# Kernel tuning notes

Hardware: AMD Instinct MI355X
Metric: run time of the kernel (lower is better)

## Reference

```python
import jax, jax.numpy as jnp
import numpy as np

B, S, HID = 8, 1024, 1024
NH, HD = 16, 64  # num heads, head dim; NH*HD == HID


def setup_inputs() -> dict:
    key = jax.random.key(0)
    ks = jax.random.split(key, 8)
    sc = 0.02
    return {
        "hidden_states": jax.random.normal(ks[0], (B, S, HID), jnp.float32),
        "attention_mask": jnp.zeros((B, 1, 1, S), jnp.float32),
        "Wq": jax.random.normal(ks[1], (HID, HID), jnp.float32) * sc,
        "bq": jnp.zeros((HID,), jnp.float32),
        "Wk": jax.random.normal(ks[2], (HID, HID), jnp.float32) * sc,
        "bk": jnp.zeros((HID,), jnp.float32),
        "Wv": jax.random.normal(ks[3], (HID, HID), jnp.float32) * sc,
        "bv": jnp.zeros((HID,), jnp.float32),
    }


def reference(hidden_states, attention_mask, Wq, bq, Wk, bk, Wv, bv):
    def split_heads(x):  # [B,S,HID] -> [B,NH,S,HD]
        return x.reshape(B, S, NH, HD).transpose(0, 2, 1, 3)

    q = split_heads(hidden_states @ Wq + bq)
    k = split_heads(hidden_states @ Wk + bk)
    v = split_heads(hidden_states @ Wv + bv)

    # [B,NH,S,S] score matrix, scale, additive mask, softmax
    scores = jnp.einsum("bhqd,bhkd->bhqk", q, k) / jnp.sqrt(jnp.float32(HD))
    scores = scores + attention_mask
    probs = jax.nn.softmax(scores, axis=-1)  # dropout prob = 0.0 -> identity

    ctx = jnp.einsum("bhqk,bhkd->bhqd", probs, v)
    return ctx.transpose(0, 2, 1, 3).reshape(B, S, HID)
```

## Files before the change

kernel.cpp:

```cpp
#include <hip/hip_runtime.h>


typedef __bf16 bf16x8 __attribute__((ext_vector_type(8)));
typedef float f32x4 __attribute__((ext_vector_type(4)));
typedef float f32x16 __attribute__((ext_vector_type(16)));
typedef int i32x4 __attribute__((ext_vector_type(4)));

__device__ __forceinline__ unsigned rne16(float x) {
  unsigned u = __builtin_bit_cast(unsigned, x);
  return (u + 0x7fffu + ((u >> 16) & 1u)) >> 16;
}
__device__ __forceinline__ unsigned packbf(float lo, float hi) {
  return rne16(lo) | (rne16(hi) << 16);
}
__device__ __forceinline__ unsigned packbf_fast(float lo, float hi) {
  unsigned ul = __builtin_bit_cast(unsigned, lo) + 0x8000u;
  unsigned uh = __builtin_bit_cast(unsigned, hi) + 0x8000u;
  return __builtin_amdgcn_perm(uh, ul, 0x07060302u);
}
__device__ __forceinline__ void async16(void* l, const void* g) {
  __builtin_amdgcn_global_load_lds((const __attribute__((address_space(1))) void*)g,
                                   (__attribute__((address_space(3))) void*)l, 16, 0, 0);
}
__device__ __forceinline__ bf16x8 dsr128(const char* p) {
  i32x4 r;
  unsigned a = (unsigned)(size_t)(const __attribute__((address_space(3))) char*)p;
  asm volatile("ds_read_b128 %0, %1" : "=v"(r) : "v"(a));
  return __builtin_bit_cast(bf16x8, r);
}

__global__ __launch_bounds__(256) void k_prep(const float* __restrict__ h,
                                              unsigned short* __restrict__ hbf,
                                              const float* __restrict__ Wq,
                                              const float* __restrict__ Wk,
                                              const float* __restrict__ Wv,
                                              unsigned short* __restrict__ wt) {
  __shared__ float t[32][33];
  int bid = blockIdx.x, tid = threadIdx.x;
  if (bid < 8192) {
    size_t i = (size_t)bid * 256 + tid;
    float4 v = ((const float4*)h)[i];
    uint2 r;
    r.x = packbf(v.x, v.y);
    r.y = packbf(v.z, v.w);
    ((uint2*)hbf)[i] = r;
  } else {
    int id = bid - 8192;
    int which = id >> 10;
    int sub = id & 1023;
    int c0 = (sub & 31) * 32, k0 = (sub >> 5) * 32;
    const float* W = which == 0 ? Wq : (which == 1 ? Wk : Wv);
    int tx = tid & 31, ty = tid >> 5;
#pragma unroll
    for (int i = 0; i < 4; ++i) {
      int r = ty + i * 8;
      t[r][tx] = W[(size_t)(k0 + r) * 1024 + c0 + tx];
    }
    __syncthreads();
#pragma unroll
    for (int i = 0; i < 4; ++i) {
      int r = ty + i * 8;
      wt[((size_t)which * 1024 + c0 + r) * 1024 + k0 + tx] = (unsigned short)rne16(t[tx][r]);
    }
  }
}

__global__ __launch_bounds__(512, 2) void k_gemm(const unsigned short* __restrict__ A,
                                                 const unsigned short* __restrict__ Bm,
                                                 const float* __restrict__ bq,
                                                 const float* __restrict__ bk,
                                                 const float* __restrict__ bv,
                                                 unsigned short* __restrict__ qkv,
                                                 unsigned short* __restrict__ vt) {
  __shared__ __align__(16) char lds[147456];
  const int tid = threadIdx.x;
  const int w = tid >> 6, lane = tid & 63;
  const int wm = w >> 1, wn = w & 1;

  int orig = blockIdx.x;
  int wgid = (orig & 7) * 96 + (orig >> 3);
  int tm = wgid / 24, tn = wgid - tm * 24;
  int m0 = tm * 256, n0 = tn * 128;

  int ro[2], ke[2];
#pragma unroll
  for (int j = 0; j < 2; ++j) {
    int o = j * 8192 + tid * 16;
    int s = o >> 10, w10 = o & 1023;
    int lg = w10 ^ (((w10 >> 9) & 1) << 5);
    ro[j] = ((s >> 1) << 4) + (lg >> 6);
    ke[j] = ((s & 1) << 5) + ((lg & 63) >> 1);
  }
  auto stage_half = [&](int ldsoff, const unsigned short* src, int rb, int k0) {
#pragma unroll
    for (int j = 0; j < 2; ++j)
      async16(lds + ldsoff + j * 8192 + w * 1024,
              src + (size_t)(rb + ro[j]) * 1024 + (k0 + ke[j]));
  };
  auto stAB = [&](int t, int doff) {
    stage_half(doff, A, m0, t * 64);
    stage_half(doff + 16384, A, m0 + 128, t * 64);
    stage_half(doff + 32768, Bm, n0, t * 64);
  };

  const int lswz = (((lane & 15) << 6) | ((lane >> 4) << 4)) ^ ((lane & 8) << 2);

  f32x4 acc[4][4];
#pragma unroll
  for (int i = 0; i < 4; ++i)
#pragma unroll
    for (int j = 0; j < 4; ++j)
#pragma unroll
      for (int e = 0; e < 4; ++e) acc[i][j][e] = 0.f;

  stAB(0, 0);
  stAB(1, 49152);
  asm volatile("s_waitcnt vmcnt(6)");
  __builtin_amdgcn_s_barrier();
  __builtin_amdgcn_sched_barrier(0);

  int cur = 0;
#pragma unroll 1
  for (int kt = 0; kt < 16; ++kt) {
    const char* buf = lds + cur * 49152;
    int nxt2 = cur + 2; if (nxt2 >= 3) nxt2 -= 3;
    const char* abase = buf + (wm >> 1) * 16384 + lswz;
    const char* bbase = buf + 32768 + lswz;
    bf16x8 aF[4][2], bF[4][2];
#pragma unroll
    for (int n = 0; n < 4; ++n)
      bF[n][0] = dsr128(bbase + ((wn * 4 + n) * 2 + 0) * 1024);
#pragma unroll
    for (int mt = 0; mt < 4; ++mt)
      aF[mt][0] = dsr128(abase + (((wm & 1) * 4 + mt) * 2 + 0) * 1024);
    if (kt < 14) stAB(kt + 2, nxt2 * 49152);
#pragma unroll
    for (int n = 0; n < 4; ++n)
      bF[n][1] = dsr128(bbase + ((wn * 4 + n) * 2 + 1) * 1024);
#pragma unroll
    for (int mt = 0; mt < 4; ++mt)
      aF[mt][1] = dsr128(abase + (((wm & 1) * 4 + mt) * 2 + 1) * 1024);
    asm volatile("s_waitcnt lgkmcnt(8)");
    __builtin_amdgcn_sched_barrier(0);
    __builtin_amdgcn_s_setprio(1);
#pragma unroll
    for (int mt = 0; mt < 4; ++mt)
#pragma unroll
      for (int n = 0; n < 4; ++n)
        acc[mt][n] = __builtin_amdgcn_mfma_f32_16x16x32_bf16(aF[mt][0], bF[n][0],
                                                             acc[mt][n], 0, 0, 0);
    __builtin_amdgcn_s_setprio(0);
    asm volatile("s_waitcnt lgkmcnt(0)");
    __builtin_amdgcn_sched_barrier(0);
    __builtin_amdgcn_s_setprio(1);
#pragma unroll
    for (int mt = 0; mt < 4; ++mt)
#pragma unroll
      for (int n = 0; n < 4; ++n)
        acc[mt][n] = __builtin_amdgcn_mfma_f32_16x16x32_bf16(aF[mt][1], bF[n][1],
                                                             acc[mt][n], 0, 0, 0);
    __builtin_amdgcn_s_setprio(0);
    if (kt < 14) asm volatile("s_waitcnt vmcnt(6)");
    else if (kt == 14) asm volatile("s_waitcnt vmcnt(0)");
    if (kt < 15) {
      __builtin_amdgcn_s_barrier();
      __builtin_amdgcn_sched_barrier(0);
    }
    cur = cur + 1; if (cur == 3) cur = 0;
  }

  const int which = tn >> 3;
  const int ng = n0 & 1023;
  const int b = m0 >> 10;
  const int r = lane & 15, qq = lane >> 4;
  const int sb = (m0 & 1023) + wm * 64 + qq * 4;

  if (which != 2) {
    const float* bp = which == 0 ? bq : bk;
    unsigned short* base = qkv + ((size_t)which << 23) + ((size_t)b << 20);
#pragma unroll
    for (int n = 0; n < 4; ++n) {
      int n_in = ng + wn * 64 + n * 16 + r;
      float bias = bp[n_in];
      unsigned short* dp = base + ((size_t)(n_in >> 6) << 16) + (n_in & 63);
#pragma unroll
      for (int m = 0; m < 4; ++m)
#pragma unroll
        for (int e = 0; e < 4; ++e)
          dp[(size_t)(sb + m * 16 + e) << 6] = (unsigned short)rne16(acc[m][n][e] + bias);
    }
  } else {
    unsigned short* vbase = vt + ((size_t)b << 20);
#pragma unroll
    for (int n = 0; n < 4; ++n) {
      int n_in = ng + wn * 64 + n * 16 + r;
      float bias = bv[n_in];
      unsigned short* dp = vbase + ((size_t)n_in << 10) + sb;
#pragma unroll
      for (int m = 0; m < 4; ++m) {
        uint2 pk;
        pk.x = packbf(acc[m][n][0] + bias, acc[m][n][1] + bias);
        pk.y = packbf(acc[m][n][2] + bias, acc[m][n][3] + bias);
        *(uint2*)(dp + m * 16) = pk;
      }
    }
  }
}

__global__ __launch_bounds__(256, 4) void k_attn(const unsigned short* __restrict__ qg,
                                                 const unsigned short* __restrict__ kg,
                                                 const unsigned short* __restrict__ vtg,
                                                 const float* __restrict__ maskg,
                                                 float* __restrict__ out) {
  __shared__ __align__(16) char lds[36864];
  char* KF = lds;
  char* VF = lds + 16384;
  float* MK = (float*)(lds + 32768);
  int tid = threadIdx.x, w = tid >> 6, lane = tid & 63, l5 = lane & 31, q5 = lane >> 5;
  int idx = blockIdx.x;
  int bi = idx & 7;
  int j = idx >> 3;
  int h = j >> 3, qc = j & 7;
  int bh = bi * 16 + h, s0 = qc * 128;
  const unsigned short* qb = qg + ((size_t)bh << 16);
  const unsigned short* kb = kg + ((size_t)bh << 16);
  const unsigned short* vb = vtg + ((size_t)bh << 16);
  const float LG = 1.4426950408889634f;
  const float C1 = 0.125f * LG;

  {
    float4 mv = *(const float4*)(maskg + (size_t)bi * 1024 + tid * 4);
    mv.x *= LG; mv.y *= LG; mv.z *= LG; mv.w *= LG;
    *(float4*)(MK + tid * 4) = mv;
  }

  bf16x8 qfr[4];
#pragma unroll
  for (int ds = 0; ds < 4; ++ds)
    qfr[ds] = *(const bf16x8*)(qb + (size_t)(s0 + w * 32 + l5) * 64 + ds * 16 + q5 * 8);

  f32x16 O[2];
#pragma unroll
  for (int i = 0; i < 2; ++i)
#pragma unroll
    for (int e = 0; e < 16; ++e) O[i][e] = 0.f;
  float lsum = 0.f;

#pragma unroll 1
  for (int kt = 0; kt < 8; ++kt) {
    int k0 = kt * 128;
    __syncthreads();
#pragma unroll
    for (int t = 0; t < 4; ++t) {
      int f = w * 4 + t, mt = f >> 2, ds = f & 3;
      async16(KF + f * 1024, kb + (size_t)(k0 + mt * 32 + l5) * 64 + ds * 16 + q5 * 8);
    }
#pragma unroll
    for (int t = 0; t < 4; ++t) {
      int f = w * 4 + t, dt = f >> 3, ks = f & 7;
      async16(VF + f * 1024, vb + (size_t)(dt * 32 + l5) * 1024 + k0 + ks * 16 + q5 * 8);
    }
    __syncthreads();

#pragma unroll
    for (int mt = 0; mt < 4; ++mt) {
      f32x16 S;
#pragma unroll
      for (int e = 0; e < 16; ++e) S[e] = 0.f;
#pragma unroll
      for (int ds = 0; ds < 4; ++ds) {
        bf16x8 a = *(const bf16x8*)(KF + (mt * 4 + ds) * 1024 + lane * 16);
        S = __builtin_amdgcn_mfma_f32_32x32x16_bf16(a, qfr[ds], S, 0, 0, 0);
      }
      float p[16];
#pragma unroll
      for (int g4 = 0; g4 < 4; ++g4) {
        float4 mv = *(const float4*)(MK + k0 + mt * 32 + g4 * 8 + q5 * 4);
        p[g4 * 4 + 0] = __builtin_amdgcn_exp2f(S[g4 * 4 + 0] * C1 + mv.x);
        p[g4 * 4 + 1] = __builtin_amdgcn_exp2f(S[g4 * 4 + 1] * C1 + mv.y);
        p[g4 * 4 + 2] = __builtin_amdgcn_exp2f(S[g4 * 4 + 2] * C1 + mv.z);
        p[g4 * 4 + 3] = __builtin_amdgcn_exp2f(S[g4 * 4 + 3] * C1 + mv.w);
      }
      unsigned p2[8];
#pragma unroll
      for (int e = 0; e < 16; ++e) lsum += p[e];
#pragma unroll
      for (int jj = 0; jj < 8; ++jj) p2[jj] = packbf_fast(p[2 * jj], p[2 * jj + 1]);
#pragma unroll
      for (int kh = 0; kh < 2; ++kh) {
        int ks = mt * 2 + kh, gp = kh * 4;
        bf16x8 av0 = *(const bf16x8*)(VF + (0 * 8 + ks) * 1024 + lane * 16);
        bf16x8 av1 = *(const bf16x8*)(VF + (1 * 8 + ks) * 1024 + lane * 16);
        unsigned o0 = p2[gp + 0], o1 = p2[gp + 1];
        unsigned o2 = p2[gp + 2], o3 = p2[gp + 3];
        unsigned t0 = __shfl_xor((int)o0, 32);
        unsigned t1 = __shfl_xor((int)o1, 32);
        unsigned t2 = __shfl_xor((int)o2, 32);
        unsigned t3 = __shfl_xor((int)o3, 32);
        uint4 fu;
        fu.x = q5 ? t2 : o0;
        fu.y = q5 ? t3 : o1;
        fu.z = q5 ? o2 : t0;
        fu.w = q5 ? o3 : t1;
        bf16x8 bfrag = __builtin_bit_cast(bf16x8, fu);
        O[0] = __builtin_amdgcn_mfma_f32_32x32x16_bf16(av0, bfrag, O[0], 0, 0, 0);
        O[1] = __builtin_amdgcn_mfma_f32_32x32x16_bf16(av1, bfrag, O[1], 0, 0, 0);
      }
    }
  }

  __syncthreads();
  float* Ob = (float*)(lds + w * 8192);
  float lt = lsum + __shfl_xor(lsum, 32);
  float rinv = 1.0f / lt;
#pragma unroll
  for (int dt = 0; dt < 2; ++dt)
#pragma unroll
    for (int g4 = 0; g4 < 4; ++g4) {
      float4 val;
      val.x = O[dt][g4 * 4 + 0] * rinv;
      val.y = O[dt][g4 * 4 + 1] * rinv;
      val.z = O[dt][g4 * 4 + 2] * rinv;
      val.w = O[dt][g4 * 4 + 3] * rinv;
      int c = dt * 8 + g4 * 2 + q5;
      *(float4*)(Ob + l5 * 64 + (c ^ (l5 & 15)) * 4) = val;
    }
#pragma unroll
  for (int t = 0; t < 8; ++t) {
    int qr = t * 4 + (lane >> 4), cr = lane & 15;
    float4 vv = *(const float4*)(Ob + qr * 64 + (cr ^ (qr & 15)) * 4);
    int s = s0 + w * 32 + qr;
    *(float4*)(out + (((size_t)(bi * 1024 + s)) << 10) + (h << 6) + (cr << 2)) = vv;
  }
}

extern "C" void kernel_launch(void* const* d_in, const int* in_sizes, int n_in,
                              void* d_out, int out_size, void* d_ws, size_t ws_size,
                              hipStream_t stream) {
  (void)in_sizes; (void)n_in; (void)out_size; (void)ws_size;
  const float* hidden = (const float*)d_in[0];
  const float* mask = (const float*)d_in[1];
  const float* Wq = (const float*)d_in[2];
  const float* bq = (const float*)d_in[3];
  const float* Wk = (const float*)d_in[4];
  const float* bk = (const float*)d_in[5];
  const float* Wv = (const float*)d_in[6];
  const float* bv = (const float*)d_in[7];
  float* out = (float*)d_out;
  char* ws = (char*)d_ws;
  unsigned short* hbf = (unsigned short*)ws;
  unsigned short* wt  = (unsigned short*)(ws + 16777216);
  unsigned short* qkv = (unsigned short*)(ws + 23068672);
  unsigned short* vt  = (unsigned short*)(ws + 56623104);

  k_prep<<<11264, 256, 0, stream>>>(hidden, hbf, Wq, Wk, Wv, wt);
  k_gemm<<<768, 512, 0, stream>>>(hbf, wt, bq, bk, bv, qkv, vt);
  k_attn<<<1024, 256, 0, stream>>>(qkv, qkv + 8388608, vt, mask, out);
}
```

Measured before the change: 215.7 us.

## Shrink QKV GEMM tile to 128x128 with 256-thread double-buffered loop

The projection GEMM moves from a 256x128 tile with 8 waves and a hand-scheduled triple-buffered LDS pipeline to a 128x128 tile with 4 waves and a plain double-buffered loop using __syncthreads. The grid doubles to 1536 blocks and LDS use drops to 64 KB, aiming for better occupancy and simpler scheduling. In exchange it gives up the explicit waitcnt/setprio interleaving and reuses each B tile across fewer A rows, which raises global and LDS traffic per FLOP.

```diff
diff --git a/kernel.cpp b/kernel.cpp
--- a/kernel.cpp
+++ b/kernel.cpp
@@ -4,7 +4,6 @@
 typedef __bf16 bf16x8 __attribute__((ext_vector_type(8)));
 typedef float f32x4 __attribute__((ext_vector_type(4)));
 typedef float f32x16 __attribute__((ext_vector_type(16)));
-typedef int i32x4 __attribute__((ext_vector_type(4)));
 
 __device__ __forceinline__ unsigned rne16(float x) {
   unsigned u = __builtin_bit_cast(unsigned, x);
@@ -21,12 +20,6 @@
 __device__ __forceinline__ void async16(void* l, const void* g) {
   __builtin_amdgcn_global_load_lds((const __attribute__((address_space(1))) void*)g,
                                    (__attribute__((address_space(3))) void*)l, 16, 0, 0);
-}
-__device__ __forceinline__ bf16x8 dsr128(const char* p) {
-  i32x4 r;
-  unsigned a = (unsigned)(size_t)(const __attribute__((address_space(3))) char*)p;
-  asm volatile("ds_read_b128 %0, %1" : "=v"(r) : "v"(a));
-  return __builtin_bit_cast(bf16x8, r);
 }
 
 __global__ __launch_bounds__(256) void k_prep(const float* __restrict__ h,
@@ -65,108 +58,83 @@
   }
 }
 
-__global__ __launch_bounds__(512, 2) void k_gemm(const unsigned short* __restrict__ A,
+__global__ __launch_bounds__(256, 2) void k_gemm(const unsigned short* __restrict__ A,
                                                  const unsigned short* __restrict__ Bm,
                                                  const float* __restrict__ bq,
                                                  const float* __restrict__ bk,
                                                  const float* __restrict__ bv,
                                                  unsigned short* __restrict__ qkv,
                                                  unsigned short* __restrict__ vt) {
-  __shared__ __align__(16) char lds[147456];
+  __shared__ __align__(16) char lds[65536];
   const int tid = threadIdx.x;
   const int w = tid >> 6, lane = tid & 63;
   const int wm = w >> 1, wn = w & 1;
 
   int orig = blockIdx.x;
-  int wgid = (orig & 7) * 96 + (orig >> 3);
+  int wgid = (orig & 7) * 192 + (orig >> 3);
   int tm = wgid / 24, tn = wgid - tm * 24;
-  int m0 = tm * 256, n0 = tn * 128;
-
-  int ro[2], ke[2];
-#pragma unroll
-  for (int j = 0; j < 2; ++j) {
-    int o = j * 8192 + tid * 16;
+  int m0 = tm * 128, n0 = tn * 128;
+
+  int ro[4], ke[4];
+#pragma unroll
+  for (int j = 0; j < 4; ++j) {
+    int o = j * 4096 + tid * 16;
     int s = o >> 10, w10 = o & 1023;
     int lg = w10 ^ (((w10 >> 9) & 1) << 5);
     ro[j] = ((s >> 1) << 4) + (lg >> 6);
     ke[j] = ((s & 1) << 5) + ((lg & 63) >> 1);
   }
-  auto stage_half = [&](int ldsoff, const unsigned short* src, int rb, int k0) {
-#pragma unroll
-    for (int j = 0; j < 2; ++j)
-      async16(lds + ldsoff + j * 8192 + w * 1024,
-              src + (size_t)(rb + ro[j]) * 1024 + (k0 + ke[j]));
+  auto stage = [&](int kt, char* buf) {
+    const unsigned short* As = A + (size_t)m0 * 1024 + kt * 64;
+    const unsigned short* Bs = Bm + (size_t)n0 * 1024 + kt * 64;
+#pragma unroll
+    for (int j = 0; j < 4; ++j) {
+      async16(buf + j * 4096 + tid * 16, As + (size_t)ro[j] * 1024 + ke[j]);
+      async16(buf + 16384 + j * 4096 + tid * 16, Bs + (size_t)ro[j] * 1024 + ke[j]);
+    }
   };
-  auto stAB = [&](int t, int doff) {
-    stage_half(doff, A, m0, t * 64);
-    stage_half(doff + 16384, A, m0 + 128, t * 64);
-    stage_half(doff + 32768, Bm, n0, t * 64);
+
+  const int lswz = (((lane & 15) << 6) | ((lane >> 4) << 4)) ^ ((lane & 8) << 2);
+
+  f32x4 acc[4][4];
+#pragma unroll
+  for (int i = 0; i < 4; ++i)
+#pragma unroll
+    for (int j = 0; j < 4; ++j)
+#pragma unroll
+      for (int e = 0; e < 4; ++e) acc[i][j][e] = 0.f;
+
+  auto compute = [&](const char* buf) {
+    const char* abase = buf + lswz;
+    const char* bbase = buf + 16384 + lswz;
+#pragma unroll
+    for (int ks = 0; ks < 2; ++ks) {
+      bf16x8 bF[4];
+#pragma unroll
+      for (int n = 0; n < 4; ++n)
+        bF[n] = *(const bf16x8*)(bbase + ((size_t)((wn * 4 + n) * 2 + ks) << 10));
+#pragma unroll
+      for (int mt = 0; mt < 4; ++mt) {
+        bf16x8 a = *(const bf16x8*)(abase + ((size_t)((wm * 4 + mt) * 2 + ks) << 10));
+#pragma unroll
+        for (int n = 0; n < 4; ++n)
+          acc[mt][n] =
+              __builtin_amdgcn_mfma_f32_16x16x32_bf16(a, bF[n], acc[mt][n], 0, 0, 0);
+      }
+    }
   };
 
-  const int lswz = (((lane & 15) << 6) | ((lane >> 4) << 4)) ^ ((lane & 8) << 2);
-
-  f32x4 acc[4][4];
-#pragma unroll
-  for (int i = 0; i < 4; ++i)
-#pragma unroll
-    for (int j = 0; j < 4; ++j)
-#pragma unroll
-      for (int e = 0; e < 4; ++e) acc[i][j][e] = 0.f;
-
-  stAB(0, 0);
-  stAB(1, 49152);
-  asm volatile("s_waitcnt vmcnt(6)");
-  __builtin_amdgcn_s_barrier();
-  __builtin_amdgcn_sched_barrier(0);
-
-  int cur = 0;
+  char* buf0 = lds;
+  char* buf1 = lds + 32768;
+  stage(0, buf0);
 #pragma unroll 1
-  for (int kt = 0; kt < 16; ++kt) {
-    const char* buf = lds + cur * 49152;
-    int nxt2 = cur + 2; if (nxt2 >= 3) nxt2 -= 3;
-    const char* abase = buf + (wm >> 1) * 16384 + lswz;
-    const char* bbase = buf + 32768 + lswz;
-    bf16x8 aF[4][2], bF[4][2];
-#pragma unroll
-    for (int n = 0; n < 4; ++n)
-      bF[n][0] = dsr128(bbase + ((wn * 4 + n) * 2 + 0) * 1024);
-#pragma unroll
-    for (int mt = 0; mt < 4; ++mt)
-      aF[mt][0] = dsr128(abase + (((wm & 1) * 4 + mt) * 2 + 0) * 1024);
-    if (kt < 14) stAB(kt + 2, nxt2 * 49152);
-#pragma unroll
-    for (int n = 0; n < 4; ++n)
-      bF[n][1] = dsr128(bbase + ((wn * 4 + n) * 2 + 1) * 1024);
-#pragma unroll
-    for (int mt = 0; mt < 4; ++mt)
-      aF[mt][1] = dsr128(abase + (((wm & 1) * 4 + mt) * 2 + 1) * 1024);
-    asm volatile("s_waitcnt lgkmcnt(8)");
-    __builtin_amdgcn_sched_barrier(0);
-    __builtin_amdgcn_s_setprio(1);
-#pragma unroll
-    for (int mt = 0; mt < 4; ++mt)
-#pragma unroll
-      for (int n = 0; n < 4; ++n)
-        acc[mt][n] = __builtin_amdgcn_mfma_f32_16x16x32_bf16(aF[mt][0], bF[n][0],
-                                                             acc[mt][n], 0, 0, 0);
-    __builtin_amdgcn_s_setprio(0);
-    asm volatile("s_waitcnt lgkmcnt(0)");
-    __builtin_amdgcn_sched_barrier(0);
-    __builtin_amdgcn_s_setprio(1);
-#pragma unroll
-    for (int mt = 0; mt < 4; ++mt)
-#pragma unroll
-      for (int n = 0; n < 4; ++n)
-        acc[mt][n] = __builtin_amdgcn_mfma_f32_16x16x32_bf16(aF[mt][1], bF[n][1],
-                                                             acc[mt][n], 0, 0, 0);
-    __builtin_amdgcn_s_setprio(0);
-    if (kt < 14) asm volatile("s_waitcnt vmcnt(6)");
-    else if (kt == 14) asm volatile("s_waitcnt vmcnt(0)");
-    if (kt < 15) {
-      __builtin_amdgcn_s_barrier();
-      __builtin_amdgcn_sched_barrier(0);
-    }
-    cur = cur + 1; if (cur == 3) cur = 0;
+  for (int kt = 0; kt < 16; kt += 2) {
+    __syncthreads();
+    stage(kt + 1, buf1);
+    compute(buf0);
+    __syncthreads();
+    if (kt + 2 < 16) stage(kt + 2, buf0);
+    compute(buf1);
   }
 
   const int which = tn >> 3;
@@ -354,6 +322,6 @@
   unsigned short* vt  = (unsigned short*)(ws + 56623104);
 
   k_prep<<<11264, 256, 0, stream>>>(hidden, hbf, Wq, Wk, Wv, wt);
-  k_gemm<<<768, 512, 0, stream>>>(hbf, wt, bq, bk, bv, qkv, vt);
+  k_gemm<<<1536, 256, 0, stream>>>(hbf, wt, bq, bk, bv, qkv, vt);
   k_attn<<<1024, 256, 0, stream>>>(qkv, qkv + 8388608, vt, mask, out);
 }
```

Result: no change. 211.9 us (-1.8%).
